# Optimization experiments

Hardware: AMD Instinct MI355X
Metric: run time of the kernel (lower is better)

## Reference

```python
import jax, jax.numpy as jnp
import numpy as np
from jax import lax

DN = ('NCDHW', 'OIDHW', 'NCDHW')
EPS = 1e-5  # torch BatchNorm1d default eps


def _cexp(v):
    # broadcast a per-channel vector over NCDHW
    return v[None, :, None, None, None]


def _bn_relu(y, g, b, rm, rv):
    inv = g * lax.rsqrt(rv + EPS)
    return jax.nn.relu((y - _cexp(rm)) * _cexp(inv) + _cexp(b))


def setup_inputs() -> dict:
    key = jax.random.key(0)
    ks = jax.random.split(key, 18)
    B, D = 2, 65
    C1, C2, CO = 1, 32, 100
    mask0 = (jax.random.uniform(ks[0], (B, 1, D, D, D)) < 0.1).astype(jnp.int32)
    x = jax.random.normal(ks[1], (B, C1, D, D, D), jnp.float32) * mask0.astype(jnp.float32)

    def w(k, shape, fan):
        return jax.random.normal(k, shape, jnp.float32) * np.float32(1.0 / np.sqrt(fan))

    return {
        'x': x, 'mask0': mask0,
        'W1': w(ks[2], (C2, C1, 3, 3, 3), C1 * 27), 'b1': w(ks[3], (C2,), C2),
        'g1': jax.random.uniform(ks[4], (C2,), jnp.float32, 0.5, 1.5),
        'bt1': w(ks[5], (C2,), C2),
        'rm1': 0.1 * jax.random.normal(ks[6], (C2,), jnp.float32),
        'rv1': jax.random.uniform(ks[7], (C2,), jnp.float32, 0.5, 1.5),
        'W2': w(ks[8], (C2, C2, 3, 3, 3), C2 * 27), 'b2': w(ks[9], (C2,), C2),
        'g2': jax.random.uniform(ks[10], (C2,), jnp.float32, 0.5, 1.5),
        'bt2': w(ks[11], (C2,), C2),
        'rm2': 0.1 * jax.random.normal(ks[12], (C2,), jnp.float32),
        'rv2': jax.random.uniform(ks[13], (C2,), jnp.float32, 0.5, 1.5),
        'Winv': w(ks[14], (CO, C2, 3, 3, 3), C2 * 27), 'binv': w(ks[15], (CO,), CO),
    }


def reference(x, mask0, W1, b1, g1, bt1, rm1, rv1,
              W2, b2, g2, bt2, rm2, rv2, Winv, binv):
    m0 = mask0.astype(x.dtype)  # [B,1,D,D,D] active input sites
    # --- SparseConv3d(1,32,k=3,s=2): dense conv is exact on zero-padded sparse features
    y1 = lax.conv_general_dilated(x, W1, (2, 2, 2), 'VALID', dimension_numbers=DN) + _cexp(b1)
    # output-active sites: any active voxel in the 3^3 receptive field
    ones_k = jnp.ones((1, 1, 3, 3, 3), x.dtype)
    cnt = lax.conv_general_dilated(m0, ones_k, (2, 2, 2), 'VALID', dimension_numbers=DN)
    m1 = (cnt > 0).astype(x.dtype)  # [B,1,Do,Do,Do]
    h1 = _bn_relu(y1, g1, bt1, rm1, rv1) * m1  # BN(eval)+ReLU only on active sites
    # --- SubMConv3d(32,32,k=3): same resolution, outputs only at active sites m1
    y2 = lax.conv_general_dilated(h1, W2, (1, 1, 1), [(1, 1)] * 3, dimension_numbers=DN) + _cexp(b2)
    h2 = _bn_relu(y2, g2, bt2, rm2, rv2) * m1
    # --- SparseInverseConv3d(32,100,k=3, indice_key='conv1'): transposed-rulebook scatter
    # back to the original conv1 input sites == stride-2 transposed conv masked by m0.
    y3 = lax.conv_general_dilated(h2, Winv, (1, 1, 1), [(2, 2)] * 3,
                                  lhs_dilation=(2, 2, 2), dimension_numbers=DN)
    out = (y3 + _cexp(binv)) * m0  # features exist only at original active voxels
    return out
```

## Files before the change

kernel.cpp:

```cpp
#include <hip/hip_runtime.h>

#define BATCH 2
#define DIN 65
#define D2IN (65*65)
#define D3IN (65*65*65)
#define NTOT (2*D3IN)
#define DO 32
#define DP 34
#define C2 32
#define CO 100
#define CAP 8192
#define EPS 1e-5f

typedef __attribute__((ext_vector_type(8))) short short8;
typedef __attribute__((ext_vector_type(4))) float floatx4;

#define H1B_OFF 0
#define H2B_OFF 1257728
#define M1_OFF  2515456
#define WB2_OFF 2580992
#define WB3_OFF 2594816
#define CNT8_OFF (2643200)
#define VOX_OFF 2643208
#define SIDX_OFF 2708744
#define RES_OFF 3258000

__device__ __forceinline__ unsigned short f2bf(float f) {
    unsigned int u = __float_as_uint(f);
    return (unsigned short)((u + 0x7fffu + ((u >> 16) & 1u)) >> 16);
}

__global__ __launch_bounds__(256) void f1(
    const float* __restrict__ x, const int* __restrict__ mask0,
    const float* __restrict__ W1, const float* __restrict__ b1,
    const float* __restrict__ g1, const float* __restrict__ bt1,
    const float* __restrict__ rm1, const float* __restrict__ rv1,
    const float* __restrict__ W2, const float* __restrict__ Winv,
    unsigned short* __restrict__ h1b, unsigned short* __restrict__ h2b,
    float* __restrict__ m1,
    unsigned short* __restrict__ wb2, unsigned short* __restrict__ wb3,
    int* __restrict__ sidx, int* __restrict__ vox, int* __restrict__ cnt8)
{
    __shared__ int lcnt[8], lbase[8];
    int bid = blockIdx.x, tid = threadIdx.x;

    if (bid < 256) {
        const int chunk = (NTOT + 255) / 256;
        int start = bid * chunk;
        int end = start + chunk; if (end > NTOT) end = NTOT;
        if (tid < 8) lcnt[tid] = 0;
        __syncthreads();
        for (int t = start + tid; t < end; t += 256) {
            if (mask0[t]) {
                int r = t % D3IN;
                int z = r / D2IN; int rem = r % D2IN;
                int y = rem / DIN; int xx = rem % DIN;
                atomicAdd(&lcnt[((z & 1) << 2) | ((y & 1) << 1) | (xx & 1)], 1);
            }
        }
        __syncthreads();
        if (tid < 8) {
            lbase[tid] = lcnt[tid] ? atomicAdd(&cnt8[tid], lcnt[tid]) : 0;
            lcnt[tid] = 0;
        }
        __syncthreads();
        for (int t = start + tid; t < end; t += 256) {
            int s = -1;
            if (mask0[t]) {
                int bb = t / D3IN; int r = t % D3IN;
                int z = r / D2IN; int rem = r % D2IN;
                int y = rem / DIN; int xx = rem % DIN;
                int cls = ((z & 1) << 2) | ((y & 1) << 1) | (xx & 1);
                int loff = atomicAdd(&lcnt[cls], 1);
                int slot = lbase[cls] + loff;
                if (slot < CAP) {
                    s = cls * CAP + slot;
                    vox[s] = (bb << 21) | (z << 14) | (y << 7) | xx;
                }
            }
            sidx[t] = s;
        }
    } else if (bid < 512) {
        int t = (bid - 256) * 256 + tid;
        int b = t >> 15, r = t & 32767;
        int z = r >> 10, y = (r >> 5) & 31, xo = r & 31;

        const float* xb = x + b * D3IN;
        const int*   mb = mask0 + b * D3IN;

        float xv[27];
        int any = 0;
#pragma unroll
        for (int kd = 0; kd < 3; kd++)
#pragma unroll
            for (int kh = 0; kh < 3; kh++)
#pragma unroll
                for (int kw = 0; kw < 3; kw++) {
                    int idx = (2 * z + kd) * D2IN + (2 * y + kh) * DIN + (2 * xo + kw);
                    xv[kd * 9 + kh * 3 + kw] = xb[idx];
                    any |= mb[idx];
                }
        float m1f = any ? 1.0f : 0.0f;
        m1[t] = m1f;

        union { unsigned short h[32]; uint4 v[4]; } u;
#pragma unroll 4
        for (int co = 0; co < 32; co++) {
            float a = 0.f;
#pragma unroll
            for (int k = 0; k < 27; k++) a += xv[k] * W1[co * 27 + k];
            float s = g1[co] * rsqrtf(rv1[co] + EPS);
            float v = (a + b1[co] - rm1[co]) * s + bt1[co];
            u.h[co] = f2bf(fmaxf(v, 0.f) * m1f);
        }
        uint4* out4 = (uint4*)(h1b + (size_t)((((b * DP + z + 1) * DP + (y + 1)) * DP + (xo + 1)) * C2));
#pragma unroll
        for (int q = 0; q < 4; q++) out4[q] = u.v[q];
    } else if (bid < 820) {
        int gid = (bid - 512) * 256 + tid;
        if (gid < 2 * 39304) {
            int b = gid / 39304; int r = gid % 39304;
            int z = r / 1156; int rem = r % 1156;
            int y = rem / 34; int xx = rem % 34;
            if (z == 0 || z == 33 || y == 0 || y == 33 || xx == 0 || xx == 33) {
                size_t off = (size_t)((((b * DP + z) * DP + y) * DP + xx) * C2);
                uint4 zv; zv.x = 0; zv.y = 0; zv.z = 0; zv.w = 0;
                uint4* p1 = (uint4*)(h1b + off);
                uint4* p2 = (uint4*)(h2b + off);
#pragma unroll
                for (int q = 0; q < 4; q++) { p1[q] = zv; p2[q] = zv; }
            }
        }
    } else {
        int gid = (bid - 820) * 256 + tid;
        if (gid < 27 * 2 * 64) {
            int q = gid;
            int tap = q >> 7, r = q & 127, ct = r >> 6, lane = r & 63;
            int n = ct * 16 + (lane & 15), kq = lane >> 4;
            union { unsigned short h[8]; uint4 v; } u;
#pragma unroll
            for (int j = 0; j < 8; j++) {
                int k = kq * 8 + j;
                u.h[j] = f2bf(W2[n * 864 + k * 27 + tap]);
            }
            *(uint4*)(wb2 + q * 8) = u.v;
        } else if (gid < 27 * 2 * 64 + 27 * 7 * 64) {
            int q = gid - 27 * 2 * 64;
            int tap = q / 448, r = q % 448, ct = r >> 6, lane = r & 63;
            int co = ct * 16 + (lane & 15), kq = lane >> 4;
            union { unsigned short h[8]; uint4 v; } u;
#pragma unroll
            for (int j = 0; j < 8; j++) {
                int k = kq * 8 + j;
                u.h[j] = (co < 100) ? f2bf(Winv[(co * 32 + k) * 27 + tap]) : (unsigned short)0;
            }
            *(uint4*)(wb3 + q * 8) = u.v;
        }
    }
}

__global__ __launch_bounds__(256) void k2(
    const unsigned short* __restrict__ h1b, const unsigned short* __restrict__ wb2,
    const float* __restrict__ b2, const float* __restrict__ g2,
    const float* __restrict__ bt2, const float* __restrict__ rm2,
    const float* __restrict__ rv2, const float* __restrict__ m1,
    unsigned short* __restrict__ h2b)
{
    int tid = threadIdx.x;
    int wv = tid >> 6, lane = tid & 63;
    int mtile = blockIdx.x * 4 + wv;
    int v0 = mtile * 16;
    int b = v0 >> 15, r = v0 & 32767;
    int z = r >> 10, y = (r >> 5) & 31, x0 = r & 31;

    int m = lane & 15, kq = lane >> 4;
    const unsigned short* abase = h1b +
        (size_t)((((b * DP + z) * DP + y) * DP + x0 + m) * C2 + kq * 8);

    floatx4 acc[2];
    acc[0] = (floatx4){0.f, 0.f, 0.f, 0.f};
    acc[1] = (floatx4){0.f, 0.f, 0.f, 0.f};

    for (int kd = 0; kd < 3; kd++)
#pragma unroll
        for (int kh = 0; kh < 3; kh++)
#pragma unroll
            for (int kw = 0; kw < 3; kw++) {
                int tap = (kd * 3 + kh) * 3 + kw;
                short8 a = *(const short8*)(abase + ((kd * DP + kh) * DP + kw) * C2);
                short8 w0 = *(const short8*)(wb2 + ((tap * 2 + 0) * 64 + lane) * 8);
                short8 w1 = *(const short8*)(wb2 + ((tap * 2 + 1) * 64 + lane) * 8);
                acc[0] = __builtin_amdgcn_mfma_f32_16x16x32_bf16(a, w0, acc[0], 0, 0, 0);
                acc[1] = __builtin_amdgcn_mfma_f32_16x16x32_bf16(a, w1, acc[1], 0, 0, 0);
            }

    float mf[4];
#pragma unroll
    for (int i = 0; i < 4; i++) mf[i] = m1[v0 + kq * 4 + i];
#pragma unroll
    for (int ct = 0; ct < 2; ct++) {
        int co = ct * 16 + m;
        float s = g2[co] * rsqrtf(rv2[co] + EPS);
        float sh = (b2[co] - rm2[co]) * s + bt2[co];
#pragma unroll
        for (int i = 0; i < 4; i++) {
            int row = kq * 4 + i;
            float val = fmaxf(acc[ct][i] * s + sh, 0.f) * mf[i];
            h2b[(size_t)((((b * DP + z + 1) * DP + (y + 1)) * DP + (x0 + row + 1)) * C2 + co)]
                = f2bf(val);
        }
    }
}

__global__ __launch_bounds__(256) void k3compute(
    const unsigned short* __restrict__ h2b, const unsigned short* __restrict__ wb3,
    const float* __restrict__ binv, const int* __restrict__ vox,
    const int* __restrict__ cnt8, float* __restrict__ res)
{
    int cls = blockIdx.y;
    int pd = (cls >> 2) & 1, ph = (cls >> 1) & 1, pw = cls & 1;
    int nh = 2 - ph, nw = 2 - pw, nhw = nh * nw;
    int ntap = (2 - pd) * nhw;
    int tid = threadIdx.x;
    int wv = tid >> 6, lane = tid & 63;
    int m = lane & 15, kq = lane >> 4;

    int n = cnt8[cls]; if (n > CAP) n = CAP;
    int ntiles = (n + 15) >> 4;

    float bv[7];
#pragma unroll
    for (int ct = 0; ct < 7; ct++) {
        int co = ct * 16 + m;
        bv[ct] = (co < 100) ? binv[co] : 0.f;
    }

    for (int t = blockIdx.x * 4 + wv; t < ntiles; t += 64 * 4) {
        int idx = t * 16 + m; if (idx >= n) idx = n - 1;
        unsigned int pv = (unsigned int)vox[cls * CAP + idx];
        int xx = pv & 127, yy = (pv >> 7) & 127, zz = (pv >> 14) & 127, bb = (pv >> 21) & 1;
        const unsigned short* abase = h2b +
            (size_t)(((((bb * DP + (zz >> 1) + pd) * DP + (yy >> 1) + ph) * DP
                       + (xx >> 1) + pw)) * C2 + kq * 8);

        floatx4 acc[7];
#pragma unroll
        for (int ct = 0; ct < 7; ct++) acc[ct] = (floatx4){0.f, 0.f, 0.f, 0.f};

        for (int tl = 0; tl < ntap; tl++) {
            int td = tl / nhw, rr = tl % nhw, th = rr / nw, tw = rr % nw;
            int tap = (pd + 2 * td) * 9 + (ph + 2 * th) * 3 + (pw + 2 * tw);
            short8 a = *(const short8*)(abase + ((td * DP + th) * DP + tw) * C2);
#pragma unroll
            for (int ct = 0; ct < 7; ct++) {
                short8 w = *(const short8*)(wb3 + ((tap * 7 + ct) * 64 + lane) * 8);
                acc[ct] = __builtin_amdgcn_mfma_f32_16x16x32_bf16(a, w, acc[ct], 0, 0, 0);
            }
        }
#pragma unroll
        for (int ct = 0; ct < 7; ct++) {
            int co = ct * 16 + m;
#pragma unroll
            for (int i = 0; i < 4; i++) {
                int ridx = t * 16 + kq * 4 + i;
                if (ridx < n)
                    res[(size_t)(cls * CAP + ridx) * 112 + co] = acc[ct][i] + bv[ct];
            }
        }
    }
}

__global__ __launch_bounds__(256) void k3write(
    const float* __restrict__ res, const int* __restrict__ sidx,
    float* __restrict__ out)
{
    __shared__ int ls[65];
    int blk = blockIdx.x;
    int y = blk % 65; int t2 = blk / 65;
    int z = t2 % 65;  int b = t2 / 65;
    int tid = threadIdx.x;
    int roff = b * D3IN + z * D2IN + y * DIN;
    if (tid < 65) ls[tid] = sidx[roff + tid];
    __syncthreads();

    int wv = tid >> 6, lane = tid & 63;
    int s = ls[lane];
    int s64 = ls[64];

    union { float4 q[7]; float f[28]; } u;
    if (s >= 0) {
        const float4* rp = (const float4*)(res + (size_t)s * 112 + wv * 28);
#pragma unroll
        for (int j = 0; j < 7; j++) u.q[j] = rp[j];
    } else {
#pragma unroll
        for (int j = 0; j < 7; j++) u.q[j] = make_float4(0.f, 0.f, 0.f, 0.f);
    }
    union { float4 q[7]; float f[28]; } u64;
    if (lane == 0) {
        if (s64 >= 0) {
            const float4* rp = (const float4*)(res + (size_t)s64 * 112 + wv * 28);
#pragma unroll
            for (int j = 0; j < 7; j++) u64.q[j] = rp[j];
        } else {
#pragma unroll
            for (int j = 0; j < 7; j++) u64.q[j] = make_float4(0.f, 0.f, 0.f, 0.f);
        }
    }

    float* obase = out + (size_t)b * 100 * D3IN + z * D2IN + y * DIN;
#pragma unroll
    for (int j = 0; j < 28; j++) {
        int co = wv * 28 + j;
        if (co < 100) {
            float* orow = obase + (size_t)co * D3IN;
            orow[lane] = u.f[j];
            if (lane == 0) orow[64] = u64.f[j];
        }
    }
}

extern "C" void kernel_launch(void* const* d_in, const int* in_sizes, int n_in,
                              void* d_out, int out_size, void* d_ws, size_t ws_size,
                              hipStream_t stream) {
    const float* x    = (const float*)d_in[0];
    const int*  mask0 = (const int*)  d_in[1];
    const float* W1   = (const float*)d_in[2];
    const float* b1   = (const float*)d_in[3];
    const float* g1   = (const float*)d_in[4];
    const float* bt1  = (const float*)d_in[5];
    const float* rm1  = (const float*)d_in[6];
    const float* rv1  = (const float*)d_in[7];
    const float* W2   = (const float*)d_in[8];
    const float* b2   = (const float*)d_in[9];
    const float* g2   = (const float*)d_in[10];
    const float* bt2  = (const float*)d_in[11];
    const float* rm2  = (const float*)d_in[12];
    const float* rv2  = (const float*)d_in[13];
    const float* Winv = (const float*)d_in[14];
    const float* binv = (const float*)d_in[15];

    float* ws = (float*)d_ws;
    unsigned short* h1b = (unsigned short*)(ws + H1B_OFF);
    unsigned short* h2b = (unsigned short*)(ws + H2B_OFF);
    float* m1   = ws + M1_OFF;
    unsigned short* wb2 = (unsigned short*)(ws + WB2_OFF);
    unsigned short* wb3 = (unsigned short*)(ws + WB3_OFF);
    int*   cnt8 = (int*)(ws + CNT8_OFF);
    int*   vox  = (int*)(ws + VOX_OFF);
    int*   sidx = (int*)(ws + SIDX_OFF);
    float* res  = ws + RES_OFF;

    hipMemsetAsync(cnt8, 0, 8 * sizeof(int), stream);

    f1<<<881, 256, 0, stream>>>(x, mask0, W1, b1, g1, bt1, rm1, rv1, W2, Winv,
                                h1b, h2b, m1, wb2, wb3, sidx, vox, cnt8);

    k2<<<1024, 256, 0, stream>>>(h1b, wb2, b2, g2, bt2, rm2, rv2, m1, h2b);

    k3compute<<<dim3(64, 8), 256, 0, stream>>>(h2b, wb3, binv, vox, cnt8, res);

    k3write<<<2 * 65 * 65, 256, 0, stream>>>(res, sidx, (float*)d_out);
}
```

Baseline: 357.0 us.

## Rewrite output writer as per-channel-plane float4 stores with padded sidx

The final write kernel now assigns one grid row per (batch, channel) output plane and has each thread emit an aligned float4 of four consecutive voxels, gathering from the result buffer via a padded per-batch sidx array. Head and tail elements that fall outside the float4 alignment are handled separately. The old writer did one row of 65 voxels per block with scalar strided stores. The mask-scan stage is also split over twice as many blocks, with cheaper batch/remainder arithmetic. The trade is fully coalesced vector stores in exchange for scattered 4-byte gathers from res, which are now repeated across 100 channel planes.

```diff
diff --git a/kernel.cpp b/kernel.cpp
--- a/kernel.cpp
+++ b/kernel.cpp
@@ -4,6 +4,7 @@
 #define DIN 65
 #define D2IN (65*65)
 #define D3IN (65*65*65)
+#define D3P 274628
 #define NTOT (2*D3IN)
 #define DO 32
 #define DP 34
@@ -39,20 +40,21 @@
     unsigned short* __restrict__ h1b, unsigned short* __restrict__ h2b,
     float* __restrict__ m1,
     unsigned short* __restrict__ wb2, unsigned short* __restrict__ wb3,
-    int* __restrict__ sidx, int* __restrict__ vox, int* __restrict__ cnt8)
+    int* __restrict__ sidxp, int* __restrict__ vox, int* __restrict__ cnt8)
 {
     __shared__ int lcnt[8], lbase[8];
     int bid = blockIdx.x, tid = threadIdx.x;
 
-    if (bid < 256) {
-        const int chunk = (NTOT + 255) / 256;
+    if (bid < 512) {
+        const int chunk = 1073;
         int start = bid * chunk;
         int end = start + chunk; if (end > NTOT) end = NTOT;
         if (tid < 8) lcnt[tid] = 0;
         __syncthreads();
         for (int t = start + tid; t < end; t += 256) {
             if (mask0[t]) {
-                int r = t % D3IN;
+                int bb = (t >= D3IN) ? 1 : 0;
+                int r = t - bb * D3IN;
                 int z = r / D2IN; int rem = r % D2IN;
                 int y = rem / DIN; int xx = rem % DIN;
                 atomicAdd(&lcnt[((z & 1) << 2) | ((y & 1) << 1) | (xx & 1)], 1);
@@ -65,9 +67,10 @@
         }
         __syncthreads();
         for (int t = start + tid; t < end; t += 256) {
+            int bb = (t >= D3IN) ? 1 : 0;
+            int r = t - bb * D3IN;
             int s = -1;
             if (mask0[t]) {
-                int bb = t / D3IN; int r = t % D3IN;
                 int z = r / D2IN; int rem = r % D2IN;
                 int y = rem / DIN; int xx = rem % DIN;
                 int cls = ((z & 1) << 2) | ((y & 1) << 1) | (xx & 1);
@@ -78,10 +81,10 @@
                     vox[s] = (bb << 21) | (z << 14) | (y << 7) | xx;
                 }
             }
-            sidx[t] = s;
-        }
-    } else if (bid < 512) {
-        int t = (bid - 256) * 256 + tid;
+            sidxp[bb * D3P + r] = s;
+        }
+    } else if (bid < 768) {
+        int t = (bid - 512) * 256 + tid;
         int b = t >> 15, r = t & 32767;
         int z = r >> 10, y = (r >> 5) & 31, xo = r & 31;
 
@@ -116,8 +119,8 @@
         uint4* out4 = (uint4*)(h1b + (size_t)((((b * DP + z + 1) * DP + (y + 1)) * DP + (xo + 1)) * C2));
 #pragma unroll
         for (int q = 0; q < 4; q++) out4[q] = u.v[q];
-    } else if (bid < 820) {
-        int gid = (bid - 512) * 256 + tid;
+    } else if (bid < 1076) {
+        int gid = (bid - 768) * 256 + tid;
         if (gid < 2 * 39304) {
             int b = gid / 39304; int r = gid % 39304;
             int z = r / 1156; int rem = r % 1156;
@@ -132,7 +135,7 @@
             }
         }
     } else {
-        int gid = (bid - 820) * 256 + tid;
+        int gid = (bid - 1076) * 256 + tid;
         if (gid < 27 * 2 * 64) {
             int q = gid;
             int tap = q >> 7, r = q & 127, ct = r >> 6, lane = r & 63;
@@ -271,51 +274,38 @@
 }
 
 __global__ __launch_bounds__(256) void k3write(
-    const float* __restrict__ res, const int* __restrict__ sidx,
+    const float* __restrict__ res, const int* __restrict__ sidxp,
     float* __restrict__ out)
 {
-    __shared__ int ls[65];
-    int blk = blockIdx.x;
-    int y = blk % 65; int t2 = blk / 65;
-    int z = t2 % 65;  int b = t2 / 65;
-    int tid = threadIdx.x;
-    int roff = b * D3IN + z * D2IN + y * DIN;
-    if (tid < 65) ls[tid] = sidx[roff + tid];
-    __syncthreads();
-
-    int wv = tid >> 6, lane = tid & 63;
-    int s = ls[lane];
-    int s64 = ls[64];
-
-    union { float4 q[7]; float f[28]; } u;
-    if (s >= 0) {
-        const float4* rp = (const float4*)(res + (size_t)s * 112 + wv * 28);
-#pragma unroll
-        for (int j = 0; j < 7; j++) u.q[j] = rp[j];
-    } else {
-#pragma unroll
-        for (int j = 0; j < 7; j++) u.q[j] = make_float4(0.f, 0.f, 0.f, 0.f);
-    }
-    union { float4 q[7]; float f[28]; } u64;
-    if (lane == 0) {
-        if (s64 >= 0) {
-            const float4* rp = (const float4*)(res + (size_t)s64 * 112 + wv * 28);
-#pragma unroll
-            for (int j = 0; j < 7; j++) u64.q[j] = rp[j];
-        } else {
-#pragma unroll
-            for (int j = 0; j < 7; j++) u64.q[j] = make_float4(0.f, 0.f, 0.f, 0.f);
-        }
-    }
-
-    float* obase = out + (size_t)b * 100 * D3IN + z * D2IN + y * DIN;
-#pragma unroll
-    for (int j = 0; j < 28; j++) {
-        int co = wv * 28 + j;
-        if (co < 100) {
-            float* orow = obase + (size_t)co * D3IN;
-            orow[lane] = u.f[j];
-            if (lane == 0) orow[64] = u64.f[j];
+    int p = blockIdx.y;
+    int b = p / 100, co = p % 100;
+    size_t plane_off = (size_t)p * D3IN;
+    size_t gs = (plane_off + 3) >> 2;
+    size_t ge = (plane_off + D3IN) >> 2;
+    const int* sb = sidxp + b * D3P;
+
+    size_t g = gs + (size_t)blockIdx.x * 256 + threadIdx.x;
+    if (g < ge) {
+        int r0 = (int)(4 * g - plane_off);
+        int s0 = sb[r0], s1 = sb[r0 + 1], s2 = sb[r0 + 2], s3 = sb[r0 + 3];
+        float4 v;
+        v.x = (s0 >= 0) ? res[(size_t)s0 * 112 + co] : 0.f;
+        v.y = (s1 >= 0) ? res[(size_t)s1 * 112 + co] : 0.f;
+        v.z = (s2 >= 0) ? res[(size_t)s2 * 112 + co] : 0.f;
+        v.w = (s3 >= 0) ? res[(size_t)s3 * 112 + co] : 0.f;
+        *(float4*)(out + 4 * g) = v;
+    }
+    if (blockIdx.x == 0) {
+        int tid = threadIdx.x;
+        int nhd = (int)(4 * gs - plane_off);
+        int ntl = (int)(plane_off + D3IN - 4 * ge);
+        if (tid < nhd) {
+            int s = sb[tid];
+            out[plane_off + tid] = (s >= 0) ? res[(size_t)s * 112 + co] : 0.f;
+        } else if (tid >= 8 && tid < 8 + ntl) {
+            int r = (int)(4 * ge - plane_off) + (tid - 8);
+            int s = sb[r];
+            out[4 * ge + (tid - 8)] = (s >= 0) ? res[(size_t)s * 112 + co] : 0.f;
         }
     }
 }
@@ -348,17 +338,17 @@
     unsigned short* wb3 = (unsigned short*)(ws + WB3_OFF);
     int*   cnt8 = (int*)(ws + CNT8_OFF);
     int*   vox  = (int*)(ws + VOX_OFF);
-    int*   sidx = (int*)(ws + SIDX_OFF);
+    int*   sidxp= (int*)(ws + SIDX_OFF);
     float* res  = ws + RES_OFF;
 
     hipMemsetAsync(cnt8, 0, 8 * sizeof(int), stream);
 
-    f1<<<881, 256, 0, stream>>>(x, mask0, W1, b1, g1, bt1, rm1, rv1, W2, Winv,
-                                h1b, h2b, m1, wb2, wb3, sidx, vox, cnt8);
+    f1<<<1137, 256, 0, stream>>>(x, mask0, W1, b1, g1, bt1, rm1, rv1, W2, Winv,
+                                 h1b, h2b, m1, wb2, wb3, sidxp, vox, cnt8);
 
     k2<<<1024, 256, 0, stream>>>(h1b, wb2, b2, g2, bt2, rm2, rv2, m1, h2b);
 
     k3compute<<<dim3(64, 8), 256, 0, stream>>>(h2b, wb3, binv, vox, cnt8, res);
 
-    k3write<<<2 * 65 * 65, 256, 0, stream>>>(res, sidx, (float*)d_out);
-}
+    k3write<<<dim3(269, 200), 256, 0, stream>>>(res, sidxp, (float*)d_out);
+}
```

Measured after the change: 436.8 us. 1.22x slower.
